# Kernel optimization log

Hardware: AMD Instinct MI355X
Metric: run time of the kernel (lower is better)

Reference implementation:

```python
import jax, jax.numpy as jnp
import numpy as np

N = 50000      # num nodes
E = 1600000    # num edges (avg degree 32)
D = 256        # in_feats
H = 256        # hidden_feats
EPS = 1e-5


def setup_inputs() -> dict:
    key = jax.random.key(0)
    ks = jax.random.split(key, 9)
    x = jax.random.normal(ks[0], (N, D), jnp.float32)
    src = jax.random.randint(ks[1], (E,), 0, N)
    dst = jax.random.randint(ks[2], (E,), 0, N)
    W1 = jax.random.normal(ks[3], (D, H), jnp.float32) / np.sqrt(D).astype(np.float32)
    b1 = jnp.zeros((H,), jnp.float32)
    W2 = jax.random.normal(ks[4], (H, H), jnp.float32) / np.sqrt(H).astype(np.float32)
    b2 = jnp.zeros((H,), jnp.float32)
    gamma = jnp.ones((H,), jnp.float32)
    beta = jnp.zeros((H,), jnp.float32)
    return {"x": x, "W1": W1, "b1": b1, "W2": W2, "b2": b2,
            "gamma": gamma, "beta": beta, "src": src, "dst": dst}


def _gcn_conv(x, src, dst, W, b):
    # DGL GraphConv with norm='both': h = D_in^{-1/2} A (D_out^{-1/2} x) W + b
    ones = jnp.ones((src.shape[0],), x.dtype)
    deg_out = jnp.maximum(jax.ops.segment_sum(ones, src, num_segments=N), 1.0)
    deg_in = jnp.maximum(jax.ops.segment_sum(ones, dst, num_segments=N), 1.0)
    h = x * (deg_out ** -0.5)[:, None]
    # project first (in >= out) to keep message width small, same math
    h = h @ W
    m = jax.ops.segment_sum(h[src], dst, num_segments=N)  # [N, H]
    return m * (deg_in ** -0.5)[:, None] + b


def _layer_norm(h, gamma, beta):
    mu = jnp.mean(h, axis=-1, keepdims=True)
    var = jnp.mean(jnp.square(h - mu), axis=-1, keepdims=True)
    return (h - mu) * jax.lax.rsqrt(var + EPS) * gamma + beta


def reference(x, W1, b1, W2, b2, gamma, beta, src, dst):
    h = _gcn_conv(x, src, dst, W1, b1)
    h = jax.nn.relu(h)
    # dropout is identity in eval mode
    h = _gcn_conv(h, src, dst, W2, b2)
    h = _layer_norm(h, gamma, beta)
    return h
```

## Files before the change

kernel.cpp:

```cpp
#include <hip/hip_runtime.h>

#define NN 50000
#define EE 1600000
#define HD 256
#define MPAD 50048
#define LN_EPS 1e-5f

#define NB 256
#define BR 196
#define NBLK 128
#define CH 12500
#define SL 16
#define SSH 12
#define FB 3136
#define FBP 3328
#define CF 13

typedef unsigned short ushort_t;
typedef unsigned int uint_t;

using frag_ab = __attribute__((ext_vector_type(8))) short;
using frag_cd = __attribute__((ext_vector_type(4))) float;

__device__ __forceinline__ ushort_t f2bf(float f) {
    uint_t u = __float_as_uint(f);
    uint_t r = (u + 0x7FFFu + ((u >> 16) & 1u)) >> 16;
    return (ushort_t)r;
}
__device__ __forceinline__ float blo(uint_t u) { return __uint_as_float(u << 16); }
__device__ __forceinline__ float bhi(uint_t u) { return __uint_as_float(u & 0xFFFF0000u); }

__global__ __launch_bounds__(256) void radix_count(
    const int* __restrict__ src, const int* __restrict__ dst,
    int* __restrict__ cntD, int* __restrict__ cntS)
{
    __shared__ int hD[NB], hS[NB];
    int t = threadIdx.x, blk = blockIdx.x;
    hD[t] = 0; hS[t] = 0;
    __syncthreads();
    for (int i = t; i < CH; i += 256) {
        int e = blk * CH + i;
        atomicAdd(&hD[dst[e] / BR], 1);
        atomicAdd(&hS[src[e] / BR], 1);
    }
    __syncthreads();
    cntD[t * NBLK + blk] = hD[t];
    cntS[t * NBLK + blk] = hS[t];
}

__global__ __launch_bounds__(256) void radix_scan(
    const int* __restrict__ cntD, int* __restrict__ scanD, int* __restrict__ bbD,
    const int* __restrict__ cntS, int* __restrict__ scanS, int* __restrict__ bbS)
{
    const int* cnt = (blockIdx.x == 0) ? cntD : cntS;
    int* scn       = (blockIdx.x == 0) ? scanD : scanS;
    int* bb        = (blockIdx.x == 0) ? bbD : bbS;
    int t = threadIdx.x, lane = t & 63, wv = t >> 6;
    int base = t * NBLK;
    int s = 0;
    for (int j = 0; j < NBLK; j++) s += cnt[base + j];
    int sc = s;
    #pragma unroll
    for (int off = 1; off < 64; off <<= 1) {
        int nv = __shfl_up(sc, off);
        if (lane >= off) sc += nv;
    }
    __shared__ int wp[4];
    if (lane == 63) wp[wv] = sc;
    __syncthreads();
    int wb = 0;
    for (int w = 0; w < wv; w++) wb += wp[w];
    int run = wb + sc - s;
    bb[t] = run;
    for (int j = 0; j < NBLK; j++) { scn[base + j] = run; run += cnt[base + j]; }
    if (t == 255) bb[256] = run;
}

__global__ __launch_bounds__(256) void radix_scatter(
    const int* __restrict__ src, const int* __restrict__ dst,
    const int* __restrict__ scanD, const int* __restrict__ scanS,
    uint2* __restrict__ dpart, int* __restrict__ spart)
{
    __shared__ int curD[NB], curS[NB];
    int t = threadIdx.x, blk = blockIdx.x;
    curD[t] = scanD[t * NBLK + blk];
    curS[t] = scanS[t * NBLK + blk];
    __syncthreads();
    for (int i = t; i < CH; i += 256) {
        int e = blk * CH + i;
        int sv = src[e], dv = dst[e];
        int pd = atomicAdd(&curD[dv / BR], 1);
        dpart[pd] = make_uint2((uint_t)sv, (uint_t)dv);
        int ps = atomicAdd(&curS[sv / BR], 1);
        spart[ps] = sv;
    }
}

__global__ __launch_bounds__(256) void fine_dst(
    const uint2* __restrict__ dpart, const int* __restrict__ bbD,
    int* __restrict__ rp16, int* __restrict__ csr_src)
{
    __shared__ int hist[FBP];
    __shared__ int cur[FBP];
    __shared__ int wp[4];
    int t = threadIdx.x, lane = t & 63, wv = t >> 6;
    int b = blockIdx.x;
    int bb = bbD[b];
    int cnt = bbD[b + 1] - bb;
    int node0 = b * BR;
    #pragma unroll
    for (int j = 0; j < CF; j++) hist[t * CF + j] = 0;
    __syncthreads();
    for (int i = t; i < cnt; i += 256) {
        uint2 p = dpart[bb + i];
        int bin = ((int)p.y - node0) * SL + ((int)p.x >> SSH);
        atomicAdd(&hist[bin], 1);
    }
    __syncthreads();
    int vals[CF];
    int s = 0;
    #pragma unroll
    for (int j = 0; j < CF; j++) { vals[j] = hist[t * CF + j]; s += vals[j]; }
    int sc = s;
    #pragma unroll
    for (int off = 1; off < 64; off <<= 1) {
        int nv = __shfl_up(sc, off);
        if (lane >= off) sc += nv;
    }
    if (lane == 63) wp[wv] = sc;
    __syncthreads();
    int wb = 0;
    for (int w = 0; w < wv; w++) wb += wp[w];
    int run = wb + sc - s;
    #pragma unroll
    for (int j = 0; j < CF; j++) {
        int bin = t * CF + j;
        cur[bin] = run;
        if (bin < FB) rp16[b * FB + bin] = bb + run;
        run += vals[j];
    }
    if (b == NB - 1 && t == 0) rp16[NB * FB] = bbD[NB];
    __syncthreads();
    for (int i = t; i < cnt; i += 256) {
        uint2 p = dpart[bb + i];
        int bin = ((int)p.y - node0) * SL + ((int)p.x >> SSH);
        int pos = bb + atomicAdd(&cur[bin], 1);
        csr_src[pos] = (int)p.x;
    }
}

__global__ __launch_bounds__(256) void fine_src(
    const int* __restrict__ spart, const int* __restrict__ bbS,
    int* __restrict__ deg_out)
{
    __shared__ int hist[NB];
    int t = threadIdx.x, b = blockIdx.x;
    hist[t] = 0;
    __syncthreads();
    int bb = bbS[b];
    int cnt = bbS[b + 1] - bb;
    int node0 = b * BR;
    for (int i = t; i < cnt; i += 256) atomicAdd(&hist[spart[bb + i] - node0], 1);
    __syncthreads();
    if (t < BR) deg_out[node0 + t] = hist[t];
}

__global__ void wconv(const float* __restrict__ W, ushort_t* __restrict__ Wt) {
    int g = blockIdx.x * 256 + threadIdx.x;
    int k = g >> 8, n = g & 255;
    Wt[n * 256 + k] = f2bf(W[g]);
}

__device__ __forceinline__ int swz(int r, int kElem) {
    return ((r * 64 + kElem) * 2) ^ ((r & 7) << 4);
}

template <int A_BF16>
__global__ __launch_bounds__(256) void gemm_mfma(
    const void* __restrict__ Aptr, const ushort_t* __restrict__ Wt,
    const int* __restrict__ deg, ushort_t* __restrict__ Y)
{
    __shared__ __align__(16) ushort_t As[8192];
    __shared__ __align__(16) ushort_t Bs[8192];
    __shared__ float sS[128];

    int t = threadIdx.x;
    int lane = t & 63, wid = t >> 6;
    int wm = wid >> 1, wn = wid & 1;
    int row0 = blockIdx.x * 128;
    int col0 = blockIdx.y * 128;

    if (t < 128) {
        int row = row0 + t;
        int dg = (row < NN) ? deg[row] : 1;
        sS[t] = rsqrtf((float)(dg > 1 ? dg : 1));
    }

    frag_cd acc[4][4];
    #pragma unroll
    for (int m = 0; m < 4; m++)
        #pragma unroll
        for (int n = 0; n < 4; n++) acc[m][n] = (frag_cd)(0.f);

    const float*    Af = (const float*)Aptr;
    const ushort_t* Ab = (const ushort_t*)Aptr;

    for (int k0 = 0; k0 < HD; k0 += 64) {
        __syncthreads();
        #pragma unroll
        for (int i = 0; i < 8; i++) {
            int flat = i * 256 + t;
            int r = flat >> 4;
            int k4 = (flat & 15) * 4;
            int row = row0 + r;
            ushort4 u;
            if constexpr (!A_BF16) {
                float4 v = make_float4(0.f, 0.f, 0.f, 0.f);
                if (row < NN) v = *(const float4*)&Af[(size_t)row * 256 + k0 + k4];
                u.x = f2bf(v.x); u.y = f2bf(v.y); u.z = f2bf(v.z); u.w = f2bf(v.w);
            } else {
                if (row < NN) u = *(const ushort4*)&Ab[(size_t)row * 256 + k0 + k4];
                else u = make_ushort4(0, 0, 0, 0);
            }
            *(ushort4*)((char*)As + swz(r, k4)) = u;
        }
        #pragma unroll
        for (int i = 0; i < 8; i++) {
            int flat = i * 256 + t;
            int nn = flat >> 4;
            int k4 = (flat & 15) * 4;
            ushort4 u = *(const ushort4*)&Wt[(size_t)(col0 + nn) * 256 + k0 + k4];
            *(ushort4*)((char*)Bs + swz(nn, k4)) = u;
        }
        __syncthreads();
        #pragma unroll
        for (int s = 0; s < 2; s++) {
            int kb = s * 32 + ((lane >> 4) * 8);
            frag_ab af[4], bfr[4];
            #pragma unroll
            for (int m = 0; m < 4; m++) {
                int r = wm * 64 + m * 16 + (lane & 15);
                af[m] = *(const frag_ab*)((const char*)As + swz(r, kb));
            }
            #pragma unroll
            for (int n = 0; n < 4; n++) {
                int c = wn * 64 + n * 16 + (lane & 15);
                bfr[n] = *(const frag_ab*)((const char*)Bs + swz(c, kb));
            }
            #pragma unroll
            for (int m = 0; m < 4; m++)
                #pragma unroll
                for (int n = 0; n < 4; n++)
                    acc[m][n] = __builtin_amdgcn_mfma_f32_16x16x32_bf16(
                        af[m], bfr[n], acc[m][n], 0, 0, 0);
        }
    }

    #pragma unroll
    for (int m = 0; m < 4; m++) {
        int rl = wm * 64 + m * 16 + ((lane >> 4) * 4);
        #pragma unroll
        for (int j = 0; j < 4; j++) {
            float sc = sS[rl + j];
            size_t grow = (size_t)(row0 + rl + j);
            #pragma unroll
            for (int n = 0; n < 4; n++) {
                int gcol = col0 + wn * 64 + n * 16 + (lane & 15);
                Y[grow * 256 + gcol] = f2bf(acc[m][n][j] * sc);
            }
        }
    }
}

template <int MODE>
__global__ __launch_bounds__(256) void aggregate_kernel(
    const ushort_t* __restrict__ msg, const int* __restrict__ rp16,
    const int* __restrict__ csr_src,
    const float* __restrict__ bias, const float* __restrict__ gamma,
    const float* __restrict__ beta, void* __restrict__ outp)
{
    int wv = threadIdx.x >> 6, lane = threadIdx.x & 63;
    int n = blockIdx.x * 4 + wv;
    if (n >= NN) return;
    int start = rp16[n * SL];
    int end   = rp16[n * SL + SL];
    int cnt = end - start;
    float a0 = 0.f, a1 = 0.f, a2 = 0.f, a3 = 0.f;
    const uint2* base = (const uint2*)msg;

    for (int c0 = 0; c0 < cnt; c0 += 64) {
        int nc = cnt - c0; if (nc > 64) nc = 64;
        int ss = csr_src[start + c0 + ((lane < nc) ? lane : 0)];
        int i = 0;
        for (; i + 16 <= nc; i += 16) {
            uint2 v[16];
            #pragma unroll
            for (int j = 0; j < 16; j++) {
                int idx = __shfl(ss, i + j);
                v[j] = base[(size_t)idx * 64 + lane];
            }
            #pragma unroll
            for (int j = 0; j < 16; j++) {
                a0 += blo(v[j].x); a1 += bhi(v[j].x);
                a2 += blo(v[j].y); a3 += bhi(v[j].y);
            }
        }
        if (i + 8 <= nc) {
            uint2 v[8];
            #pragma unroll
            for (int j = 0; j < 8; j++) {
                int idx = __shfl(ss, i + j);
                v[j] = base[(size_t)idx * 64 + lane];
            }
            #pragma unroll
            for (int j = 0; j < 8; j++) {
                a0 += blo(v[j].x); a1 += bhi(v[j].x);
                a2 += blo(v[j].y); a3 += bhi(v[j].y);
            }
            i += 8;
        }
        if (i + 4 <= nc) {
            uint2 v[4];
            #pragma unroll
            for (int j = 0; j < 4; j++) {
                int idx = __shfl(ss, i + j);
                v[j] = base[(size_t)idx * 64 + lane];
            }
            #pragma unroll
            for (int j = 0; j < 4; j++) {
                a0 += blo(v[j].x); a1 += bhi(v[j].x);
                a2 += blo(v[j].y); a3 += bhi(v[j].y);
            }
            i += 4;
        }
        for (; i < nc; i++) {
            int idx = __shfl(ss, i);
            uint2 v = base[(size_t)idx * 64 + lane];
            a0 += blo(v.x); a1 += bhi(v.x); a2 += blo(v.y); a3 += bhi(v.y);
        }
    }

    float scl = rsqrtf((float)(cnt > 1 ? cnt : 1));
    float4 b = ((const float4*)bias)[lane];
    float r0 = a0 * scl + b.x;
    float r1 = a1 * scl + b.y;
    float r2 = a2 * scl + b.z;
    float r3 = a3 * scl + b.w;

    if (MODE == 0) {
        r0 = fmaxf(r0, 0.f); r1 = fmaxf(r1, 0.f);
        r2 = fmaxf(r2, 0.f); r3 = fmaxf(r3, 0.f);
        uint2 o;
        o.x = (uint_t)f2bf(r0) | ((uint_t)f2bf(r1) << 16);
        o.y = (uint_t)f2bf(r2) | ((uint_t)f2bf(r3) << 16);
        ((uint2*)outp)[(size_t)n * 64 + lane] = o;
    } else {
        float s1 = r0 + r1 + r2 + r3;
        #pragma unroll
        for (int off = 1; off < 64; off <<= 1) s1 += __shfl_xor(s1, off);
        float mu = s1 * (1.f / 256.f);
        float d0 = r0 - mu, d1 = r1 - mu, d2 = r2 - mu, d3 = r3 - mu;
        float s2 = d0 * d0 + d1 * d1 + d2 * d2 + d3 * d3;
        #pragma unroll
        for (int off = 1; off < 64; off <<= 1) s2 += __shfl_xor(s2, off);
        float rs = rsqrtf(s2 * (1.f / 256.f) + LN_EPS);
        float4 g  = ((const float4*)gamma)[lane];
        float4 be = ((const float4*)beta)[lane];
        float4 o;
        o.x = d0 * rs * g.x + be.x;
        o.y = d1 * rs * g.y + be.y;
        o.z = d2 * rs * g.z + be.z;
        o.w = d3 * rs * g.w + be.w;
        ((float4*)outp)[(size_t)n * 64 + lane] = o;
    }
}

extern "C" void kernel_launch(void* const* d_in, const int* in_sizes, int n_in,
                              void* d_out, int out_size, void* d_ws, size_t ws_size,
                              hipStream_t stream)
{
    const float* x     = (const float*)d_in[0];
    const float* W1    = (const float*)d_in[1];
    const float* b1    = (const float*)d_in[2];
    const float* W2    = (const float*)d_in[3];
    const float* b2    = (const float*)d_in[4];
    const float* gamma = (const float*)d_in[5];
    const float* beta  = (const float*)d_in[6];
    const int*   src   = (const int*)d_in[7];
    const int*   dst   = (const int*)d_in[8];
    float* out = (float*)d_out;

    uint2*    dpart  = (uint2*)d_ws;
    ushort_t* msg    = (ushort_t*)(dpart + EE);
    int*      csr    = (int*)(msg + (size_t)MPAD * 256);
    int*      spart  = csr + EE;
    int*      rp16   = spart + EE;
    int*      cntD   = rp16 + NB * FB + 16;
    int*      cntS   = cntD + NB * NBLK;
    int*      scanD  = cntS + NB * NBLK;
    int*      scanS  = scanD + NB * NBLK;
    int*      bbD    = scanS + NB * NBLK;
    int*      bbS    = bbD + 320;
    int*      degout = bbS + 320;
    ushort_t* Wt1    = (ushort_t*)(degout + NB * BR);
    ushort_t* Wt2    = Wt1 + 65536;

    ushort_t* h = (ushort_t*)d_out;

    radix_count  <<<NBLK, 256, 0, stream>>>(src, dst, cntD, cntS);
    radix_scan   <<<2, 256, 0, stream>>>(cntD, scanD, bbD, cntS, scanS, bbS);
    radix_scatter<<<NBLK, 256, 0, stream>>>(src, dst, scanD, scanS, dpart, spart);
    fine_dst     <<<NB, 256, 0, stream>>>(dpart, bbD, rp16, csr);
    fine_src     <<<NB, 256, 0, stream>>>(spart, bbS, degout);

    wconv<<<256, 256, 0, stream>>>(W1, Wt1);
    wconv<<<256, 256, 0, stream>>>(W2, Wt2);

    dim3 gg(MPAD / 128, 2);
    gemm_mfma<0><<<gg, 256, 0, stream>>>(x, Wt1, degout, msg);
    aggregate_kernel<0><<<(NN + 3) / 4, 256, 0, stream>>>(msg, rp16, csr,
                                                          b1, nullptr, nullptr, h);
    gemm_mfma<1><<<gg, 256, 0, stream>>>(h, Wt2, degout, msg);
    aggregate_kernel<1><<<(NN + 3) / 4, 256, 0, stream>>>(msg, rp16, csr,
                                                          b2, gamma, beta, out);
}
```

Measured before the change: 485.5 us.

## Use FP8 messages for layer one, pack dst partition, retile GEMM to full width

Layer-one messages are stored as FP8 e4m3 instead of bf16, which halves the gather traffic in the first aggregation, and a dedicated fp8 aggregate kernel decodes them. Other changes: the radix count uses per-wave histograms to cut LDS atomic contention, the dst partition is packed into 32 bits (src in the low 16 bits, local dst in the high bits), the two weight conversions are merged into one launch, and the GEMM uses 64-row tiles covering all 256 columns. FP8 quantization of messages loses accuracy and may exceed tolerance. Packing src into 16 bits truncates node ids at or above 65536, which is safe only because N is 50000.

New measurement: 424.8 us. -12.5%, faster.

```diff
diff --git a/kernel.cpp b/kernel.cpp
--- a/kernel.cpp
+++ b/kernel.cpp
@@ -1,4 +1,5 @@
 #include <hip/hip_runtime.h>
+#include <hip/hip_fp8.h>
 
 #define NN 50000
 #define EE 1600000
@@ -8,6 +9,7 @@
 
 #define NB 256
 #define BR 196
+#define NTOT (NB * BR)
 #define NBLK 128
 #define CH 12500
 #define SL 16
@@ -18,6 +20,7 @@
 
 typedef unsigned short ushort_t;
 typedef unsigned int uint_t;
+typedef unsigned char uchar_t;
 
 using frag_ab = __attribute__((ext_vector_type(8))) short;
 using frag_cd = __attribute__((ext_vector_type(4))) float;
@@ -30,22 +33,33 @@
 __device__ __forceinline__ float blo(uint_t u) { return __uint_as_float(u << 16); }
 __device__ __forceinline__ float bhi(uint_t u) { return __uint_as_float(u & 0xFFFF0000u); }
 
+__device__ __forceinline__ uchar_t f2fp8(float f) {
+    __hip_fp8_e4m3 q(f);
+    return (uchar_t)q.__x;
+}
+__device__ __forceinline__ float fp8f(uint_t byte) {
+    __hip_fp8_e4m3 t;
+    t.__x = (__hip_fp8_storage_t)byte;
+    return (float)t;
+}
+
 __global__ __launch_bounds__(256) void radix_count(
     const int* __restrict__ src, const int* __restrict__ dst,
     int* __restrict__ cntD, int* __restrict__ cntS)
 {
-    __shared__ int hD[NB], hS[NB];
-    int t = threadIdx.x, blk = blockIdx.x;
-    hD[t] = 0; hS[t] = 0;
+    __shared__ int hD[4][NB], hS[4][NB];
+    int t = threadIdx.x, blk = blockIdx.x, wv = t >> 6;
+    #pragma unroll
+    for (int w = 0; w < 4; w++) { hD[w][t] = 0; hS[w][t] = 0; }
     __syncthreads();
     for (int i = t; i < CH; i += 256) {
         int e = blk * CH + i;
-        atomicAdd(&hD[dst[e] / BR], 1);
-        atomicAdd(&hS[src[e] / BR], 1);
-    }
-    __syncthreads();
-    cntD[t * NBLK + blk] = hD[t];
-    cntS[t * NBLK + blk] = hS[t];
+        atomicAdd(&hD[wv][dst[e] / BR], 1);
+        atomicAdd(&hS[wv][src[e] / BR], 1);
+    }
+    __syncthreads();
+    cntD[t * NBLK + blk] = hD[0][t] + hD[1][t] + hD[2][t] + hD[3][t];
+    cntS[t * NBLK + blk] = hS[0][t] + hS[1][t] + hS[2][t] + hS[3][t];
 }
 
 __global__ __launch_bounds__(256) void radix_scan(
@@ -79,7 +93,7 @@
 __global__ __launch_bounds__(256) void radix_scatter(
     const int* __restrict__ src, const int* __restrict__ dst,
     const int* __restrict__ scanD, const int* __restrict__ scanS,
-    uint2* __restrict__ dpart, int* __restrict__ spart)
+    uint_t* __restrict__ dpart, int* __restrict__ spart)
 {
     __shared__ int curD[NB], curS[NB];
     int t = threadIdx.x, blk = blockIdx.x;
@@ -89,15 +103,17 @@
     for (int i = t; i < CH; i += 256) {
         int e = blk * CH + i;
         int sv = src[e], dv = dst[e];
-        int pd = atomicAdd(&curD[dv / BR], 1);
-        dpart[pd] = make_uint2((uint_t)sv, (uint_t)dv);
+        int bk = dv / BR;
+        int ld = dv - bk * BR;
+        int pd = atomicAdd(&curD[bk], 1);
+        dpart[pd] = (uint_t)sv | ((uint_t)ld << 16);
         int ps = atomicAdd(&curS[sv / BR], 1);
         spart[ps] = sv;
     }
 }
 
 __global__ __launch_bounds__(256) void fine_dst(
-    const uint2* __restrict__ dpart, const int* __restrict__ bbD,
+    const uint_t* __restrict__ dpart, const int* __restrict__ bbD,
     int* __restrict__ rp16, int* __restrict__ csr_src)
 {
     __shared__ int hist[FBP];
@@ -107,14 +123,14 @@
     int b = blockIdx.x;
     int bb = bbD[b];
     int cnt = bbD[b + 1] - bb;
-    int node0 = b * BR;
     #pragma unroll
     for (int j = 0; j < CF; j++) hist[t * CF + j] = 0;
     __syncthreads();
     for (int i = t; i < cnt; i += 256) {
-        uint2 p = dpart[bb + i];
-        int bin = ((int)p.y - node0) * SL + ((int)p.x >> SSH);
-        atomicAdd(&hist[bin], 1);
+        uint_t p = dpart[bb + i];
+        int sv = (int)(p & 0xFFFFu);
+        int ld = (int)(p >> 16);
+        atomicAdd(&hist[ld * SL + (sv >> SSH)], 1);
     }
     __syncthreads();
     int vals[CF];
@@ -142,10 +158,11 @@
     if (b == NB - 1 && t == 0) rp16[NB * FB] = bbD[NB];
     __syncthreads();
     for (int i = t; i < cnt; i += 256) {
-        uint2 p = dpart[bb + i];
-        int bin = ((int)p.y - node0) * SL + ((int)p.x >> SSH);
-        int pos = bb + atomicAdd(&cur[bin], 1);
-        csr_src[pos] = (int)p.x;
+        uint_t p = dpart[bb + i];
+        int sv = (int)(p & 0xFFFFu);
+        int ld = (int)(p >> 16);
+        int pos = bb + atomicAdd(&cur[ld * SL + (sv >> SSH)], 1);
+        csr_src[pos] = sv;
     }
 }
 
@@ -165,8 +182,12 @@
     if (t < BR) deg_out[node0 + t] = hist[t];
 }
 
-__global__ void wconv(const float* __restrict__ W, ushort_t* __restrict__ Wt) {
-    int g = blockIdx.x * 256 + threadIdx.x;
+__global__ void wconv2(const float* __restrict__ W1, const float* __restrict__ W2,
+                       ushort_t* __restrict__ Wt1, ushort_t* __restrict__ Wt2) {
+    int b = blockIdx.x;
+    const float* W = (b < 256) ? W1 : W2;
+    ushort_t* Wt   = (b < 256) ? Wt1 : Wt2;
+    int g = (b & 255) * 256 + threadIdx.x;
     int k = g >> 8, n = g & 255;
     Wt[n * 256 + k] = f2bf(W[g]);
 }
@@ -175,22 +196,20 @@
     return ((r * 64 + kElem) * 2) ^ ((r & 7) << 4);
 }
 
-template <int A_BF16>
+template <int A_BF16, int OUT_FP8>
 __global__ __launch_bounds__(256) void gemm_mfma(
     const void* __restrict__ Aptr, const ushort_t* __restrict__ Wt,
-    const int* __restrict__ deg, ushort_t* __restrict__ Y)
-{
-    __shared__ __align__(16) ushort_t As[8192];
-    __shared__ __align__(16) ushort_t Bs[8192];
-    __shared__ float sS[128];
+    const int* __restrict__ deg, void* __restrict__ Yp)
+{
+    __shared__ __align__(16) ushort_t As[4096];
+    __shared__ __align__(16) ushort_t Bs[16384];
+    __shared__ float sS[64];
 
     int t = threadIdx.x;
-    int lane = t & 63, wid = t >> 6;
-    int wm = wid >> 1, wn = wid & 1;
-    int row0 = blockIdx.x * 128;
-    int col0 = blockIdx.y * 128;
-
-    if (t < 128) {
+    int lane = t & 63, wn = t >> 6;
+    int row0 = blockIdx.x * 64;
+
+    if (t < 64) {
         int row = row0 + t;
         int dg = (row < NN) ? deg[row] : 1;
         sS[t] = rsqrtf((float)(dg > 1 ? dg : 1));
@@ -208,7 +227,7 @@
     for (int k0 = 0; k0 < HD; k0 += 64) {
         __syncthreads();
         #pragma unroll
-        for (int i = 0; i < 8; i++) {
+        for (int i = 0; i < 4; i++) {
             int flat = i * 256 + t;
             int r = flat >> 4;
             int k4 = (flat & 15) * 4;
@@ -225,11 +244,11 @@
             *(ushort4*)((char*)As + swz(r, k4)) = u;
         }
         #pragma unroll
-        for (int i = 0; i < 8; i++) {
+        for (int i = 0; i < 16; i++) {
             int flat = i * 256 + t;
             int nn = flat >> 4;
             int k4 = (flat & 15) * 4;
-            ushort4 u = *(const ushort4*)&Wt[(size_t)(col0 + nn) * 256 + k0 + k4];
+            ushort4 u = *(const ushort4*)&Wt[(size_t)nn * 256 + k0 + k4];
             *(ushort4*)((char*)Bs + swz(nn, k4)) = u;
         }
         __syncthreads();
@@ -239,7 +258,7 @@
             frag_ab af[4], bfr[4];
             #pragma unroll
             for (int m = 0; m < 4; m++) {
-                int r = wm * 64 + m * 16 + (lane & 15);
+                int r = m * 16 + (lane & 15);
                 af[m] = *(const frag_ab*)((const char*)As + swz(r, kb));
             }
             #pragma unroll
@@ -258,26 +277,107 @@
 
     #pragma unroll
     for (int m = 0; m < 4; m++) {
-        int rl = wm * 64 + m * 16 + ((lane >> 4) * 4);
+        int rl = m * 16 + ((lane >> 4) * 4);
         #pragma unroll
         for (int j = 0; j < 4; j++) {
             float sc = sS[rl + j];
             size_t grow = (size_t)(row0 + rl + j);
             #pragma unroll
             for (int n = 0; n < 4; n++) {
-                int gcol = col0 + wn * 64 + n * 16 + (lane & 15);
-                Y[grow * 256 + gcol] = f2bf(acc[m][n][j] * sc);
-            }
-        }
-    }
-}
-
-template <int MODE>
-__global__ __launch_bounds__(256) void aggregate_kernel(
+                int gcol = wn * 64 + n * 16 + (lane & 15);
+                if constexpr (OUT_FP8) {
+                    ((uchar_t*)Yp)[grow * 256 + gcol] = f2fp8(acc[m][n][j] * sc);
+                } else {
+                    ((ushort_t*)Yp)[grow * 256 + gcol] = f2bf(acc[m][n][j] * sc);
+                }
+            }
+        }
+    }
+}
+
+__global__ __launch_bounds__(256) void aggregate_fp8(
+    const uint_t* __restrict__ msg, const int* __restrict__ rp16,
+    const int* __restrict__ csr_src, const float* __restrict__ bias,
+    void* __restrict__ outp)
+{
+    int wv = threadIdx.x >> 6, lane = threadIdx.x & 63;
+    int n = blockIdx.x * 4 + wv;
+    if (n >= NN) return;
+    int start = rp16[n * SL];
+    int end   = rp16[n * SL + SL];
+    int cnt = end - start;
+    float a0 = 0.f, a1 = 0.f, a2 = 0.f, a3 = 0.f;
+
+    for (int c0 = 0; c0 < cnt; c0 += 64) {
+        int nc = cnt - c0; if (nc > 64) nc = 64;
+        int ss = csr_src[start + c0 + ((lane < nc) ? lane : 0)];
+        int i = 0;
+        for (; i + 16 <= nc; i += 16) {
+            uint_t v[16];
+            #pragma unroll
+            for (int j = 0; j < 16; j++) {
+                int idx = __shfl(ss, i + j);
+                v[j] = msg[(size_t)idx * 64 + lane];
+            }
+            #pragma unroll
+            for (int j = 0; j < 16; j++) {
+                a0 += fp8f(v[j] & 0xFFu);         a1 += fp8f((v[j] >> 8) & 0xFFu);
+                a2 += fp8f((v[j] >> 16) & 0xFFu); a3 += fp8f(v[j] >> 24);
+            }
+        }
+        if (i + 8 <= nc) {
+            uint_t v[8];
+            #pragma unroll
+            for (int j = 0; j < 8; j++) {
+                int idx = __shfl(ss, i + j);
+                v[j] = msg[(size_t)idx * 64 + lane];
+            }
+            #pragma unroll
+            for (int j = 0; j < 8; j++) {
+                a0 += fp8f(v[j] & 0xFFu);         a1 += fp8f((v[j] >> 8) & 0xFFu);
+                a2 += fp8f((v[j] >> 16) & 0xFFu); a3 += fp8f(v[j] >> 24);
+            }
+            i += 8;
+        }
+        if (i + 4 <= nc) {
+            uint_t v[4];
+            #pragma unroll
+            for (int j = 0; j < 4; j++) {
+                int idx = __shfl(ss, i + j);
+                v[j] = msg[(size_t)idx * 64 + lane];
+            }
+            #pragma unroll
+            for (int j = 0; j < 4; j++) {
+                a0 += fp8f(v[j] & 0xFFu);         a1 += fp8f((v[j] >> 8) & 0xFFu);
+                a2 += fp8f((v[j] >> 16) & 0xFFu); a3 += fp8f(v[j] >> 24);
+            }
+            i += 4;
+        }
+        for (; i < nc; i++) {
+            int idx = __shfl(ss, i);
+            uint_t v = msg[(size_t)idx * 64 + lane];
+            a0 += fp8f(v & 0xFFu);         a1 += fp8f((v >> 8) & 0xFFu);
+            a2 += fp8f((v >> 16) & 0xFFu); a3 += fp8f(v >> 24);
+        }
+    }
+
+    float scl = rsqrtf((float)(cnt > 1 ? cnt : 1));
+    float4 b = ((const float4*)bias)[lane];
+    float r0 = fmaxf(a0 * scl + b.x, 0.f);
+    float r1 = fmaxf(a1 * scl + b.y, 0.f);
+    float r2 = fmaxf(a2 * scl + b.z, 0.f);
+    float r3 = fmaxf(a3 * scl + b.w, 0.f);
+    uint2 o;
+    o.x = (uint_t)f2bf(r0) | ((uint_t)f2bf(r1) << 16);
+    o.y = (uint_t)f2bf(r2) | ((uint_t)f2bf(r3) << 16);
+    ((uint2*)outp)[(size_t)n * 64 + lane] = o;
+}
+
+__global__ __launch_bounds__(256) void aggregate_bf16(
     const ushort_t* __restrict__ msg, const int* __restrict__ rp16,
-    const int* __restrict__ csr_src,
-    const float* __restrict__ bias, const float* __restrict__ gamma,
-    const float* __restrict__ beta, void* __restrict__ outp)
+    const int* __restrict__ csr_src, const float* __restrict__ bias,
+    const float* __restrict__ gamma, const float* __restrict__ beta,
+    float* __restrict__ outp)
 {
     int wv = threadIdx.x >> 6, lane = threadIdx.x & 63;
     int n = blockIdx.x * 4 + wv;
@@ -347,32 +447,23 @@
     float r2 = a2 * scl + b.z;
     float r3 = a3 * scl + b.w;
 
-    if (MODE == 0) {
-        r0 = fmaxf(r0, 0.f); r1 = fmaxf(r1, 0.f);
-        r2 = fmaxf(r2, 0.f); r3 = fmaxf(r3, 0.f);
-        uint2 o;
-        o.x = (uint_t)f2bf(r0) | ((uint_t)f2bf(r1) << 16);
-        o.y = (uint_t)f2bf(r2) | ((uint_t)f2bf(r3) << 16);
-        ((uint2*)outp)[(size_t)n * 64 + lane] = o;
-    } else {
-        float s1 = r0 + r1 + r2 + r3;
-        #pragma unroll
-        for (int off = 1; off < 64; off <<= 1) s1 += __shfl_xor(s1, off);
-        float mu = s1 * (1.f / 256.f);
-        float d0 = r0 - mu, d1 = r1 - mu, d2 = r2 - mu, d3 = r3 - mu;
-        float s2 = d0 * d0 + d1 * d1 + d2 * d2 + d3 * d3;
-        #pragma unroll
-        for (int off = 1; off < 64; off <<= 1) s2 += __shfl_xor(s2, off);
-        float rs = rsqrtf(s2 * (1.f / 256.f) + LN_EPS);
-        float4 g  = ((const float4*)gamma)[lane];
-        float4 be = ((const float4*)beta)[lane];
-        float4 o;
-        o.x = d0 * rs * g.x + be.x;
-        o.y = d1 * rs * g.y + be.y;
-        o.z = d2 * rs * g.z + be.z;
-        o.w = d3 * rs * g.w + be.w;
-        ((float4*)outp)[(size_t)n * 64 + lane] = o;
-    }
+    float s1 = r0 + r1 + r2 + r3;
+    #pragma unroll
+    for (int off = 1; off < 64; off <<= 1) s1 += __shfl_xor(s1, off);
+    float mu = s1 * (1.f / 256.f);
+    float d0 = r0 - mu, d1 = r1 - mu, d2 = r2 - mu, d3 = r3 - mu;
+    float s2 = d0 * d0 + d1 * d1 + d2 * d2 + d3 * d3;
+    #pragma unroll
+    for (int off = 1; off < 64; off <<= 1) s2 += __shfl_xor(s2, off);
+    float rs = rsqrtf(s2 * (1.f / 256.f) + LN_EPS);
+    float4 g  = ((const float4*)gamma)[lane];
+    float4 be = ((const float4*)beta)[lane];
+    float4 o;
+    o.x = d0 * rs * g.x + be.x;
+    o.y = d1 * rs * g.y + be.y;
+    o.z = d2 * rs * g.z + be.z;
+    o.w = d3 * rs * g.w + be.w;
+    ((float4*)&outp[(size_t)n * 256])[lane] = o;
 }
 
 extern "C" void kernel_launch(void* const* d_in, const int* in_sizes, int n_in,
@@ -390,20 +481,22 @@
     const int*   dst   = (const int*)d_in[8];
     float* out = (float*)d_out;
 
-    uint2*    dpart  = (uint2*)d_ws;
-    ushort_t* msg    = (ushort_t*)(dpart + EE);
-    int*      csr    = (int*)(msg + (size_t)MPAD * 256);
-    int*      spart  = csr + EE;
-    int*      rp16   = spart + EE;
-    int*      cntD   = rp16 + NB * FB + 16;
+    char* base = (char*)d_ws;
+    uchar_t*  msg8   = (uchar_t*)base;
+    uint_t*   dpart  = (uint_t*)base;
+    int*      spart  = (int*)(base + 6400000);
+    int*      csr    = (int*)(base + 12812288);
+    int*      rp16   = (int*)(base + 19212288);
+    int*      cntD   = (int*)(base + 22423680);
     int*      cntS   = cntD + NB * NBLK;
     int*      scanD  = cntS + NB * NBLK;
     int*      scanS  = scanD + NB * NBLK;
     int*      bbD    = scanS + NB * NBLK;
     int*      bbS    = bbD + 320;
     int*      degout = bbS + 320;
-    ushort_t* Wt1    = (ushort_t*)(degout + NB * BR);
+    ushort_t* Wt1    = (ushort_t*)(degout + NTOT);
     ushort_t* Wt2    = Wt1 + 65536;
+    ushort_t* msg16  = Wt2 + 65536;
 
     ushort_t* h = (ushort_t*)d_out;
 
@@ -412,15 +505,12 @@
     radix_scatter<<<NBLK, 256, 0, stream>>>(src, dst, scanD, scanS, dpart, spart);
     fine_dst     <<<NB, 256, 0, stream>>>(dpart, bbD, rp16, csr);
     fine_src     <<<NB, 256, 0, stream>>>(spart, bbS, degout);
-
-    wconv<<<256, 256, 0, stream>>>(W1, Wt1);
-    wconv<<<256, 256, 0, stream>>>(W2, Wt2);
-
-    dim3 gg(MPAD / 128, 2);
-    gemm_mfma<0><<<gg, 256, 0, stream>>>(x, Wt1, degout, msg);
-    aggregate_kernel<0><<<(NN + 3) / 4, 256, 0, stream>>>(msg, rp16, csr,
-                                                          b1, nullptr, nullptr, h);
-    gemm_mfma<1><<<gg, 256, 0, stream>>>(h, Wt2, degout, msg);
-    aggregate_kernel<1><<<(NN + 3) / 4, 256, 0, stream>>>(msg, rp16, csr,
-                                                          b2, gamma, beta, out);
-}
+    wconv2       <<<512, 256, 0, stream>>>(W1, W2, Wt1, Wt2);
+
+    gemm_mfma<0, 1><<<MPAD / 64, 256, 0, stream>>>(x, Wt1, degout, msg8);
+    aggregate_fp8<<<(NN + 3) / 4, 256, 0, stream>>>((const uint_t*)msg8, rp16, csr,
+                                                    b1, h);
+    gemm_mfma<1, 0><<<MPAD / 64, 256, 0, stream>>>(h, Wt2, degout, msg16);
+    aggregate_bf16<<<(NN + 3) / 4, 256, 0, stream>>>(msg16, rp16, csr,
+                                                     b2, gamma, beta, out);
+}
```
